# Optimization experiments

Hardware: AMD Instinct MI355X
Metric: run time of the kernel (lower is better)

## Reference

```python
import jax, jax.numpy as jnp
import numpy as np

N_ELEM = 10   # len(EnvPara.ELEMENTS)
N_ATOMS = 100000
N_DIM = 256


def setup_inputs() -> dict:
    key = jax.random.key(0)
    k = jax.random.split(key, 5)
    return {
        "input_tensor": jax.random.normal(k[0], (N_ATOMS, N_DIM), jnp.float32),
        "species": jax.random.randint(k[1], (N_ATOMS,), 0, N_ELEM, dtype=jnp.int64),
        "W1": jax.random.normal(k[2], (N_ELEM, N_DIM, N_DIM), jnp.float32) / np.sqrt(N_DIM).astype(np.float32),
        "b1": jnp.zeros((N_ELEM, N_DIM), jnp.float32),
        "W2": jax.random.normal(k[3], (N_ELEM, N_DIM, 1), jnp.float32) / np.sqrt(N_DIM).astype(np.float32),
        "b2": jnp.zeros((N_ELEM, 1), jnp.float32),
    }


def _element_linear(x, species, W, b):
    # Species-routed linear: each atom uses the weight/bias of its element.
    # Loop over the small fixed element set (N_ELEM=10) to avoid materializing
    # a [n_atoms, d_in, d_out] gathered-weight tensor.
    out = jnp.zeros((x.shape[0], W.shape[2]), dtype=x.dtype)
    for e in range(W.shape[0]):
        mask = (species == e)[:, None]                      # [n_atoms, 1]
        out = out + jnp.where(mask, x @ W[e] + b[e], jnp.zeros((), x.dtype))
    return out


def reference(input_tensor, species, W1, b1, W2, b2):
    # layer2(silu(layer1(x)))
    h = _element_linear(input_tensor, species, W1, b1)      # [n_atoms, n_dim]
    h = jax.nn.silu(h)                                      # way=0 -> plain SiLU
    return _element_linear(h, species, W2, b2)              # [n_atoms, 1]
```

## Files before the change

### kernel.cpp

```cpp
#include <hip/hip_runtime.h>
#include <hip/hip_bf16.h>
#include <stdint.h>


#define NDIM 256
#define CHUNKS 16
#define BCHUNK 16384
#define TROWS 64
#define MAXT 16
#define NB_GEMM 256

typedef __attribute__((ext_vector_type(8))) short short8;
typedef __attribute__((ext_vector_type(8))) unsigned short ushort8;
typedef __attribute__((ext_vector_type(4))) float f32x4;
typedef __attribute__((ext_vector_type(2))) unsigned u32x2;

__device__ __forceinline__ unsigned short f2bf(float f) {
  unsigned u = __float_as_uint(f);
  u = (u + 0x7FFFu + ((u >> 16) & 1u)) >> 16;
  return (unsigned short)u;
}

__device__ __forceinline__ unsigned pk2(float a, float b) {
  return (unsigned)f2bf(a) | ((unsigned)f2bf(b) << 16);
}


__global__ void convw_k(const float* __restrict__ W1, unsigned short* __restrict__ wt, int NE) {
  __shared__ float ldsW[32 * 260];
  int blk = blockIdx.x;
  int e = blk >> 3, step = blk & 7;
  int tid = threadIdx.x;
  int k0 = step * 32;
  {
    int kk = tid >> 3, part = tid & 7;
    const float* src = W1 + ((size_t)e << 16) + (size_t)(k0 + kk) * NDIM + part * 32;
    #pragma unroll
    for (int j = 0; j < 8; ++j) {
      float4 v = *(const float4*)(src + j * 4);
      *(float4*)&ldsW[kk * 260 + part * 32 + j * 4] = v;
    }
  }
  __syncthreads();
  {
    int n = tid;
    unsigned short v[32];
    #pragma unroll
    for (int kk = 0; kk < 32; ++kk) v[kk] = f2bf(ldsW[kk * 260 + n]);
    char* chunk = (char*)wt + (size_t)blk * BCHUNK;
    unsigned swz = (unsigned)((n & 7) << 4);
    #pragma unroll
    for (int g = 0; g < 4; ++g)
      *(ushort8*)(chunk + (((unsigned)(n * 64 + g * 16)) ^ swz)) = *(ushort8*)&v[g * 8];
  }
}

__global__ void bhist_k(const int* __restrict__ sp, int n, int* __restrict__ bc, int NE) {
  __shared__ int wc[4][16];
  int tid = threadIdx.x;
  int i = blockIdx.x * 256 + tid;
  int s = (i < n) ? sp[i] : -1;
  int w = tid >> 6, lane = tid & 63;
  for (int e = 0; e < NE; ++e) {
    unsigned long long m = __ballot(s == e);
    if (lane == 0) wc[w][e] = __popcll(m);
  }
  __syncthreads();
  if (tid < NE) bc[blockIdx.x * NE + tid] = wc[0][tid] + wc[1][tid] + wc[2][tid] + wc[3][tid];
}

__global__ void scan_k(const int* __restrict__ bc, int* __restrict__ bo,
                       int* __restrict__ atom_start, int* __restrict__ tile_off,
                       int* __restrict__ bstart, int nblocks, int NE) {
  __shared__ int csum[256];
  __shared__ int coff[256];
  __shared__ int stot[16];
  __shared__ int sbase[16];
  int tid = threadIdx.x;
  int per = (nblocks + CHUNKS - 1) / CHUNKS;
  int e = tid / CHUNKS, c = tid % CHUNKS;
  int b0 = c * per, b1 = b0 + per; if (b1 > nblocks) b1 = nblocks;
  if (tid < NE * CHUNKS) {
    int s = 0;
    for (int b = b0; b < b1; ++b) s += bc[b * NE + e];
    csum[tid] = s;
  }
  __syncthreads();
  if (tid < NE) {
    int r = 0;
    for (int c2 = 0; c2 < CHUNKS; ++c2) { coff[tid * CHUNKS + c2] = r; r += csum[tid * CHUNKS + c2]; }
    stot[tid] = r;
  }
  __syncthreads();
  if (tid == 0) {
    int a = 0, t = 0;
    for (int e2 = 0; e2 < NE; ++e2) {
      sbase[e2] = a;
      atom_start[e2] = a; tile_off[e2] = t;
      a += stot[e2]; t += (stot[e2] + TROWS - 1) / TROWS;
    }
    atom_start[NE] = a; tile_off[NE] = t;
    int ntl = t > 0 ? t : 1;
    int nbk[16]; int tot = 0, emax = 0;
    for (int e2 = 0; e2 < NE; ++e2) {
      int nt = tile_off[e2 + 1] - tile_off[e2];
      int v = (nt > 0) ? (int)(((long long)nt * NB_GEMM) / ntl) : 0;
      if (nt > 0 && v < 1) v = 1;
      nbk[e2] = v; tot += v;
      if (nbk[e2] > nbk[emax]) emax = e2;
    }
    nbk[emax] += NB_GEMM - tot;
    int bacc = 0;
    for (int e2 = 0; e2 < NE; ++e2) { bstart[e2] = bacc; bacc += nbk[e2]; }
    bstart[NE] = bacc;
  }
  __syncthreads();
  if (tid < NE * CHUNKS) {
    int run = sbase[e] + coff[tid];
    for (int b = b0; b < b1; ++b) { bo[b * NE + e] = run; run += bc[b * NE + e]; }
  }
}

__global__ void dscatter_k(const int* __restrict__ sp, int n, const int* __restrict__ bo,
                           int* __restrict__ sorted, int NE) {
  __shared__ int wc[4][16];
  int tid = threadIdx.x;
  int i = blockIdx.x * 256 + tid;
  int s = (i < n) ? sp[i] : -1;
  int w = tid >> 6, lane = tid & 63;
  for (int e = 0; e < NE; ++e) {
    unsigned long long m = __ballot(s == e);
    if (lane == 0) wc[w][e] = __popcll(m);
  }
  __syncthreads();
  for (int e = 0; e < NE; ++e) {
    unsigned long long m = __ballot(s == e);
    if (s == e) {
      int wpre = 0;
      for (int w2 = 0; w2 < 4; ++w2) if (w2 < w) wpre += wc[w2][e];
      int rank = __popcll(m & ((1ull << lane) - 1ull));
      sorted[bo[blockIdx.x * NE + e] + wpre + rank] = i;
    }
  }
}


__global__ __launch_bounds__(512, 1) void gemm_k(
    const float* __restrict__ x, const unsigned short* __restrict__ wt,
    const float* __restrict__ b1, const float* __restrict__ w2,
    const float* __restrict__ b2, const int* __restrict__ sorted,
    const int* __restrict__ atom_start, const int* __restrict__ tile_off,
    const int* __restrict__ bstart, float* __restrict__ out, int NE)
{
  __shared__ __align__(16) char ldsT[TROWS * 512];
  __shared__ float partLds[8 * TROWS];
  __shared__ int ldsAtoms[MAXT * TROWS];
  __shared__ int toffs[17], astart[17], bst[17];

  int tid = threadIdx.x, lane = tid & 63, wid = tid >> 6;
  int lr = lane & 15, lg = lane >> 4;

  if (tid <= NE) {
    toffs[tid] = tile_off[tid]; astart[tid] = atom_start[tid]; bst[tid] = bstart[tid];
  }
  __syncthreads();

  int b = blockIdx.x;
  int e = 0;
  while (b >= bst[e + 1]) ++e;
  int j = b - bst[e], nbe = bst[e + 1] - bst[e];
  int nte = toffs[e + 1] - toffs[e];
  int q = nte / nbe, r = nte % nbe;
  int cnt = q + (j < r ? 1 : 0);
  if (cnt <= 0) return;
  if (cnt > MAXT) cnt = MAXT;
  int t0 = toffs[e] + j * q + (j < r ? j : r);
  int t1 = t0 + cnt;

  {
    int rs0 = astart[e] + (t0 - toffs[e]) * TROWS;
    int rvAll = astart[e + 1] - rs0;
    for (int i = tid; i < cnt * TROWS; i += 512) {
      int rloc = (i < rvAll) ? i : (rvAll - 1);
      ldsAtoms[i] = sorted[rs0 + rloc];
    }
  }
  __syncthreads();

  short8 bf[2][8];
  float bbv[2][4], wvv[2][4];
  {
    const char* wbase = (const char*)wt + (size_t)e * 8 * BCHUNK;
    #pragma unroll
    for (int mf = 0; mf < 2; ++mf) {
      int ncol = wid * 32 + mf * 16 + lr;
      unsigned off = ((unsigned)(ncol * 64 + lg * 16)) ^ ((unsigned)((ncol & 7) << 4));
      #pragma unroll
      for (int s = 0; s < 8; ++s)
        bf[mf][s] = *(const short8*)(wbase + (size_t)s * BCHUNK + off);
      #pragma unroll
      for (int rg = 0; rg < 4; ++rg) {
        int n = wid * 32 + mf * 16 + lg * 4 + rg;
        bbv[mf][rg] = b1[(size_t)e * NDIM + n];
        wvv[mf][rg] = w2[(size_t)e * NDIM + n];
      }
    }
  }
  float b2v = b2[e];
  #pragma unroll
  for (int mf = 0; mf < 2; ++mf)
    #pragma unroll
    for (int s = 0; s < 8; ++s) asm volatile("" : "+v"(bf[mf][s]));

  int srow = tid >> 3;
  int skc  = tid & 7;
  unsigned swzW = (unsigned)((srow & 7) << 4);
  float4 xr[8];
  {
    int atom = ldsAtoms[srow];
    const float* xp = x + (size_t)atom * NDIM + skc * 4;
    #pragma unroll
    for (int jj = 0; jj < 8; ++jj) xr[jj] = *(const float4*)(xp + jj * 32);
  }

  for (int t = t0; t < t1; ++t) {
    #pragma unroll
    for (int jj = 0; jj < 8; ++jj) {
      u32x2 w;
      w[0] = pk2(xr[jj].x, xr[jj].y); w[1] = pk2(xr[jj].z, xr[jj].w);
      *(u32x2*)(ldsT + (((unsigned)(srow * 512 + jj * 64 + skc * 8)) ^ swzW)) = w;
    }
    if (t + 1 < t1) {
      int atom = ldsAtoms[(t + 1 - t0) * TROWS + srow];
      const float* xp = x + (size_t)atom * NDIM + skc * 4;
      #pragma unroll
      for (int jj = 0; jj < 8; ++jj) xr[jj] = *(const float4*)(xp + jj * 32);
    }

    asm volatile("s_waitcnt lgkmcnt(0)" ::: "memory");
    __builtin_amdgcn_s_barrier();
    __builtin_amdgcn_sched_barrier(0);

    f32x4 acc[2][4];
    const f32x4 zero = {0.f, 0.f, 0.f, 0.f};
    #pragma unroll
    for (int i = 0; i < 2; ++i)
      #pragma unroll
      for (int jj = 0; jj < 4; ++jj) acc[i][jj] = zero;

    #pragma unroll
    for (int step = 0; step < 8; ++step) {
      short8 af[4];
      #pragma unroll
      for (int nf = 0; nf < 4; ++nf) {
        unsigned off = ((unsigned)((nf * 16 + lr) * 512 + step * 64 + lg * 16))
                     ^ ((unsigned)((lr & 7) << 4));
        af[nf] = *(const short8*)(ldsT + off);
      }
      #pragma unroll
      for (int mf = 0; mf < 2; ++mf)
        #pragma unroll
        for (int nf = 0; nf < 4; ++nf)
          acc[mf][nf] = __builtin_amdgcn_mfma_f32_16x16x32_bf16(bf[mf][step], af[nf], acc[mf][nf], 0, 0, 0);
    }

    float p[4];
    #pragma unroll
    for (int nf = 0; nf < 4; ++nf) {
      float s = 0.f;
      #pragma unroll
      for (int mf = 0; mf < 2; ++mf)
        #pragma unroll
        for (int rg = 0; rg < 4; ++rg) {
          float h = acc[mf][nf][rg] + bbv[mf][rg];
          s += h * __builtin_amdgcn_rcpf(1.f + __expf(-h)) * wvv[mf][rg];
        }
      s += __shfl_xor(s, 16, 64);
      s += __shfl_xor(s, 32, 64);
      p[nf] = s;
    }
    if (lg == 0) {
      #pragma unroll
      for (int nf = 0; nf < 4; ++nf)
        partLds[wid * TROWS + nf * 16 + lr] = p[nf];
    }

    asm volatile("s_waitcnt lgkmcnt(0)" ::: "memory");
    __builtin_amdgcn_s_barrier();
    __builtin_amdgcn_sched_barrier(0);

    if (tid < TROWS) {
      float s = b2v;
      #pragma unroll
      for (int w = 0; w < 8; ++w) s += partLds[w * TROWS + tid];
      out[ldsAtoms[(t - t0) * TROWS + tid]] = s;
    }
  }
}


extern "C" void kernel_launch(void* const* d_in, const int* in_sizes, int n_in,
                              void* d_out, int out_size, void* d_ws, size_t ws_size,
                              hipStream_t stream) {
  const float* x  = (const float*)d_in[0];
  const int*   sp = (const int*)d_in[1];
  const float* W1 = (const float*)d_in[2];
  const float* b1 = (const float*)d_in[3];
  const float* W2 = (const float*)d_in[4];
  const float* b2 = (const float*)d_in[5];
  float* out = (float*)d_out;

  int n_atoms = in_sizes[0] / NDIM;
  int NE = in_sizes[2] / (NDIM * NDIM);
  int nblocks = (n_atoms + 255) / 256;

  char* wsb = (char*)d_ws;
  size_t o = 0;
  int* bc = (int*)(wsb + o);         o += ((size_t)nblocks * NE * 4 + 255) & ~(size_t)255;
  int* bo = (int*)(wsb + o);         o += ((size_t)nblocks * NE * 4 + 255) & ~(size_t)255;
  int* atom_start = (int*)(wsb + o); o += 256;
  int* tile_off   = (int*)(wsb + o); o += 256;
  int* bstart     = (int*)(wsb + o); o += 256;
  int* sorted     = (int*)(wsb + o); o += ((size_t)n_atoms * 4 + 255) & ~(size_t)255;
  unsigned short* wt = (unsigned short*)(wsb + o);

  hipLaunchKernelGGL(convw_k, dim3(NE * 8), dim3(256), 0, stream, W1, wt, NE);
  hipLaunchKernelGGL(bhist_k, dim3(nblocks), dim3(256), 0, stream, sp, n_atoms, bc, NE);
  hipLaunchKernelGGL(scan_k, dim3(1), dim3(256), 0, stream, bc, bo, atom_start, tile_off,
                     bstart, nblocks, NE);
  hipLaunchKernelGGL(dscatter_k, dim3(nblocks), dim3(256), 0, stream, sp, n_atoms, bo,
                     sorted, NE);

  hipLaunchKernelGGL(gemm_k, dim3(NB_GEMM), dim3(512), 0, stream,
                     x, wt, b1, W2, b2, sorted, atom_start, tile_off, bstart, out, NE);
}
```

Before: 61.12 us.

## Raise occupancy to two blocks per CU and stage bias/W2 in LDS

Sets launch bounds to allow two 512-thread blocks per CU. To cut register pressure, the per-lane b1 and w2 values move from registers into shared memory and are reread as vectors in the epilogue. The weight fragments are now loaded with inline-asm global loads plus an explicit vmcnt wait. The aim is more latency hiding from higher occupancy, at the cost of extra LDS reads per tile and possible register spills under the tighter 128-VGPR budget.

```diff
diff --git a/kernel.cpp b/kernel.cpp
--- a/kernel.cpp
+++ b/kernel.cpp
@@ -145,7 +145,7 @@
 }
 
 
-__global__ __launch_bounds__(512, 1) void gemm_k(
+__global__ __launch_bounds__(512, 2) void gemm_k(
     const float* __restrict__ x, const unsigned short* __restrict__ wt,
     const float* __restrict__ b1, const float* __restrict__ w2,
     const float* __restrict__ b2, const int* __restrict__ sorted,
@@ -154,6 +154,7 @@
 {
   __shared__ __align__(16) char ldsT[TROWS * 512];
   __shared__ float partLds[8 * TROWS];
+  __shared__ __align__(16) float b1s[NDIM], w2s[NDIM];
   __shared__ int ldsAtoms[MAXT * TROWS];
   __shared__ int toffs[17], astart[17], bst[17];
 
@@ -184,11 +185,13 @@
       int rloc = (i < rvAll) ? i : (rvAll - 1);
       ldsAtoms[i] = sorted[rs0 + rloc];
     }
-  }
-  __syncthreads();
+    if (tid < NDIM) {
+      b1s[tid] = b1[(size_t)e * NDIM + tid];
+      w2s[tid] = w2[(size_t)e * NDIM + tid];
+    }
+  }
 
   short8 bf[2][8];
-  float bbv[2][4], wvv[2][4];
   {
     const char* wbase = (const char*)wt + (size_t)e * 8 * BCHUNK;
     #pragma unroll
@@ -196,21 +199,16 @@
       int ncol = wid * 32 + mf * 16 + lr;
       unsigned off = ((unsigned)(ncol * 64 + lg * 16)) ^ ((unsigned)((ncol & 7) << 4));
       #pragma unroll
-      for (int s = 0; s < 8; ++s)
-        bf[mf][s] = *(const short8*)(wbase + (size_t)s * BCHUNK + off);
-      #pragma unroll
-      for (int rg = 0; rg < 4; ++rg) {
-        int n = wid * 32 + mf * 16 + lg * 4 + rg;
-        bbv[mf][rg] = b1[(size_t)e * NDIM + n];
-        wvv[mf][rg] = w2[(size_t)e * NDIM + n];
+      for (int s = 0; s < 8; ++s) {
+        const char* p = wbase + (size_t)s * BCHUNK + off;
+        asm volatile("global_load_dwordx4 %0, %1, off"
+                     : "=v"(bf[mf][s]) : "v"(p));
       }
     }
+    asm volatile("s_waitcnt vmcnt(0)" ::: "memory");
   }
   float b2v = b2[e];
-  #pragma unroll
-  for (int mf = 0; mf < 2; ++mf)
-    #pragma unroll
-    for (int s = 0; s < 8; ++s) asm volatile("" : "+v"(bf[mf][s]));
+  __syncthreads();
 
   int srow = tid >> 3;
   int skc  = tid & 7;
@@ -269,12 +267,15 @@
     for (int nf = 0; nf < 4; ++nf) {
       float s = 0.f;
       #pragma unroll
-      for (int mf = 0; mf < 2; ++mf)
+      for (int mf = 0; mf < 2; ++mf) {
+        f32x4 bb = *(const f32x4*)&b1s[wid * 32 + mf * 16 + lg * 4];
+        f32x4 wv = *(const f32x4*)&w2s[wid * 32 + mf * 16 + lg * 4];
         #pragma unroll
         for (int rg = 0; rg < 4; ++rg) {
-          float h = acc[mf][nf][rg] + bbv[mf][rg];
-          s += h * __builtin_amdgcn_rcpf(1.f + __expf(-h)) * wvv[mf][rg];
+          float h = acc[mf][nf][rg] + bb[rg];
+          s += h * __builtin_amdgcn_rcpf(1.f + __expf(-h)) * wv[rg];
         }
+      }
       s += __shfl_xor(s, 16, 64);
       s += __shfl_xor(s, 32, 64);
       p[nf] = s;
```

New measurement: 61.52 us. About the same (+0.6%).
